# Performance work log

Hardware: AMD Instinct MI355X
Metric: run time of the kernel (lower is better)

Reference implementation:

```python
import jax, jax.numpy as jnp
import numpy as np

B, T, C = 4, 2048, 2048
H, KV, HD = 16, 4, 128  # n_head, n_kv_head, head_dim
G = H // KV             # query heads per kv head


def _rope(t, cos, sin):
    # t: [B, T, h, HD]; cos/sin: [T, HD//2] -> broadcast as [1, T, 1, HD//2]
    tr = t.reshape(t.shape[:-1] + (HD // 2, 2))
    t_r, t_i = tr[..., 0], tr[..., 1]
    c = cos[None, :, None, :]
    s = sin[None, :, None, :]
    o_r = t_r * c - t_i * s
    o_i = t_r * s + t_i * c
    return jnp.stack((o_r, o_i), axis=-1).reshape(t.shape)


def setup_inputs() -> dict:
    key = jax.random.key(0)
    ks = jax.random.split(key, 7)
    sc = 0.02
    return {
        "x": jax.random.normal(ks[0], (B, T, C), jnp.float32),
        "cos_freqs": jnp.cos(jnp.outer(jnp.arange(T, dtype=jnp.float32),
                                       1.0 / (10000.0 ** (jnp.arange(HD // 2, dtype=jnp.float32) * 2 / HD)))),
        "sin_freqs": jnp.sin(jnp.outer(jnp.arange(T, dtype=jnp.float32),
                                       1.0 / (10000.0 ** (jnp.arange(HD // 2, dtype=jnp.float32) * 2 / HD)))),
        "wq": jax.random.normal(ks[1], (H * HD, C), jnp.float32) * sc,
        "wk": jax.random.normal(ks[2], (KV * HD, C), jnp.float32) * sc,
        "wv": jax.random.normal(ks[3], (KV * HD, C), jnp.float32) * sc,
        "wo": jax.random.normal(ks[4], (C, H * HD), jnp.float32) * sc,
    }


def reference(x, cos_freqs, sin_freqs, wq, wk, wv, wo):
    # projections (Linear with bias=False: y = x @ W.T)
    q = (x @ wq.T).reshape(B, T, H, HD)
    k = (x @ wk.T).reshape(B, T, KV, HD)
    v = (x @ wv.T).reshape(B, T, KV, HD)
    q, k = _rope(q, cos_freqs, sin_freqs), _rope(k, cos_freqs, sin_freqs)
    # GQA attention without materializing repeated K/V: group q heads per kv head
    qg = q.reshape(B, T, KV, G, HD).transpose(0, 2, 3, 1, 4)  # [B,KV,G,T,HD]
    kh = k.transpose(0, 2, 1, 3)                              # [B,KV,T,HD]
    vh = v.transpose(0, 2, 1, 3)                              # [B,KV,T,HD]
    scale = 1.0 / jnp.sqrt(jnp.float32(HD))
    scores = jnp.einsum('bkgtd,bksd->bkgts', qg, kh) * scale  # [B,KV,G,T,T]
    mask = jnp.tril(jnp.ones((T, T), dtype=bool))
    scores = jnp.where(mask, scores, jnp.float32(-jnp.inf))
    attn = jax.nn.softmax(scores, axis=-1)
    out = jnp.einsum('bkgts,bksd->bkgtd', attn, vh)           # [B,KV,G,T,HD]
    out = out.transpose(0, 3, 1, 2, 4).reshape(B, T, H * HD)
    return out @ wo.T
```

## Files before the change

### kernel.cpp

```cpp
#include <hip/hip_runtime.h>
#include <hip/hip_bf16.h>
#include <math.h>

typedef __attribute__((ext_vector_type(8))) short short8;
typedef __attribute__((ext_vector_type(4))) float floatx4;

__device__ __forceinline__ float bf2f(unsigned short u) {
  union { unsigned int i; float f; } x; x.i = ((unsigned int)u) << 16; return x.f;
}
__device__ __forceinline__ unsigned short f2bf(float f) {
  union { float f; unsigned int i; } x; x.f = f;
  unsigned int r = x.i + 0x7FFFu + ((x.i >> 16) & 1u);
  return (unsigned short)(r >> 16);
}
__device__ __forceinline__ unsigned int pack2bf(float a, float b) {
  return (unsigned int)f2bf(a) | ((unsigned int)f2bf(b) << 16);
}
__device__ __forceinline__ void gl16(const void* g, void* l) {
  __builtin_amdgcn_global_load_lds(
      (const __attribute__((address_space(1))) unsigned int*)g,
      (__attribute__((address_space(3))) unsigned int*)l, 16, 0, 0);
}
#define BARF  do { __builtin_amdgcn_s_barrier(); asm volatile("" ::: "memory"); } while (0)

__global__ void cvt_f32_bf16(const float* __restrict__ in, unsigned short* __restrict__ out, int n4) {
  int i = blockIdx.x * blockDim.x + threadIdx.x;
  if (i >= n4) return;
  float4 v = ((const float4*)in)[i];
  ushort4 o;
  o.x = f2bf(v.x); o.y = f2bf(v.y); o.z = f2bf(v.z); o.w = f2bf(v.w);
  ((ushort4*)out)[i] = o;
}

template<int MODE>
__global__ __launch_bounds__(512, 2) void gemm_bt(const unsigned short* __restrict__ A,
                                                  const unsigned short* __restrict__ Bw,
                                                  void* __restrict__ out0,
                                                  unsigned short* __restrict__ vtg,
                                                  int M, int N, int K, int nbx) {
  extern __shared__ unsigned short SM[];
  const int nb = gridDim.x;
  const int bid = blockIdx.x;
  const int tile = (bid & 7) * (nb >> 3) + (bid >> 3);
  const int n0 = (tile % nbx) * 256, m0 = (tile / nbx) * 256;
  const int tid = threadIdx.x;
  const int lane = tid & 63, wave = tid >> 6;
  const int wm = wave >> 2, wn = wave & 3;
  const int r = lane & 15, g = lane >> 4;
  const int rh = r >> 1;
  const int slot = (((r & 1) << 2) | g) ^ rh;

  const int sg8 = (tid & 7) ^ ((tid >> 3) & 7);
  const int srow = 2 * (tid >> 3) + (sg8 >> 2);
  const int scol = (sg8 & 3) * 8;
  const unsigned short* Agb = A  + (size_t)(m0 + srow) * K + scol;
  const unsigned short* Bgb = Bw + (size_t)(n0 + srow) * K + scol;
  const size_t K128 = (size_t)K * 128;
  char* const SMb = (char*)SM;

  const int aob = (wm * 64 + rh) * 64 + slot * 8;
  const int bob = 16384 + (wn * 32 + rh) * 64 + slot * 8;

  auto STA = [&](int s, int t, int kh) {
    const unsigned short* gp = Agb + ((size_t)t << 6) + kh * 32;
    char* d = SMb + s * 65536 + kh * 16384 + wave * 1024;
    gl16(gp,        d);
    gl16(gp + K128, d + 8192);
  };
  auto STB = [&](int s, int t, int kh) {
    const unsigned short* gp = Bgb + ((size_t)t << 6) + kh * 32;
    char* d = SMb + s * 65536 + 32768 + kh * 16384 + wave * 1024;
    gl16(gp,        d);
    gl16(gp + K128, d + 8192);
  };

  floatx4 acc[8][4] = {};
  const int NT = K >> 6;

  STA(0, 0, 0); STB(0, 0, 0);
  STA(0, 0, 1); STB(0, 0, 1);
  asm volatile("s_waitcnt vmcnt(0)" ::: "memory");
  __builtin_amdgcn_s_barrier();
  asm volatile("" ::: "memory");

  short8 bfrA[4], afA[4];
#pragma unroll
  for (int j = 0; j < 4; ++j) bfrA[j] = *(const short8*)&SM[bob + j * 512];
#pragma unroll
  for (int i = 0; i < 4; ++i) afA[i] = *(const short8*)&SM[aob + i * 512];

  for (int t = 0; t < NT; ++t) {
    const int s = t & 1;
    const unsigned short* Ls = SM + s * 32768;
    const unsigned short* Ln = SM + (s ^ 1) * 32768;
    const bool pf = (t + 1 < NT);
    short8 afB[4], bfrB[4], afA2[4], afB2[4];

#pragma unroll
    for (int i = 0; i < 4; ++i) afB[i] = *(const short8*)&Ls[aob + (4 + i) * 512];
    if (pf) { STA(s ^ 1, t + 1, 0); STB(s ^ 1, t + 1, 0); }
    __builtin_amdgcn_s_setprio(1);
#pragma unroll
    for (int i = 0; i < 4; ++i)
#pragma unroll
      for (int j = 0; j < 4; ++j)
        acc[i][j] = __builtin_amdgcn_mfma_f32_16x16x32_bf16(afA[i], bfrA[j], acc[i][j], 0, 0, 0);
    __builtin_amdgcn_s_setprio(0);

#pragma unroll
    for (int j = 0; j < 4; ++j) bfrB[j] = *(const short8*)&Ls[bob + 8192 + j * 512];
#pragma unroll
    for (int i = 0; i < 4; ++i) afA2[i] = *(const short8*)&Ls[aob + 8192 + i * 512];
    if (pf) { STA(s ^ 1, t + 1, 1); STB(s ^ 1, t + 1, 1); }
    __builtin_amdgcn_s_setprio(1);
#pragma unroll
    for (int i = 0; i < 4; ++i)
#pragma unroll
      for (int j = 0; j < 4; ++j)
        acc[4 + i][j] = __builtin_amdgcn_mfma_f32_16x16x32_bf16(afB[i], bfrA[j], acc[4 + i][j], 0, 0, 0);
    __builtin_amdgcn_s_setprio(0);

#pragma unroll
    for (int i = 0; i < 4; ++i) afB2[i] = *(const short8*)&Ls[aob + 8192 + (4 + i) * 512];
    __builtin_amdgcn_s_setprio(1);
#pragma unroll
    for (int i = 0; i < 4; ++i)
#pragma unroll
      for (int j = 0; j < 4; ++j)
        acc[i][j] = __builtin_amdgcn_mfma_f32_16x16x32_bf16(afA2[i], bfrB[j], acc[i][j], 0, 0, 0);
    __builtin_amdgcn_s_setprio(0);

    asm volatile("s_waitcnt lgkmcnt(0)" ::: "memory");
    if (pf) asm volatile("s_waitcnt vmcnt(0)" ::: "memory");
    __builtin_amdgcn_s_barrier();
    asm volatile("" ::: "memory");
    if (pf) {
#pragma unroll
      for (int j = 0; j < 4; ++j) bfrA[j] = *(const short8*)&Ln[bob + j * 512];
#pragma unroll
      for (int i = 0; i < 4; ++i) afA[i] = *(const short8*)&Ln[aob + i * 512];
    }
    __builtin_amdgcn_s_setprio(1);
#pragma unroll
    for (int i = 0; i < 4; ++i)
#pragma unroll
      for (int j = 0; j < 4; ++j)
        acc[4 + i][j] = __builtin_amdgcn_mfma_f32_16x16x32_bf16(afB2[i], bfrB[j], acc[4 + i][j], 0, 0, 0);
    __builtin_amdgcn_s_setprio(0);
  }

  if (MODE == 0) {
    float* SMf = (float*)SM;
    float* outp = (float*)out0;
#pragma unroll
    for (int sp = 0; sp < 4; ++sp) {
      __syncthreads();
      if (wn == sp) {
#pragma unroll
        for (int i = 0; i < 8; ++i)
#pragma unroll
          for (int j = 0; j < 4; ++j)
#pragma unroll
            for (int q = 0; q < 4; ++q)
              SMf[(wm * 128 + i * 16 + g * 4 + q) * 64 + j * 16 + r] = acc[i][j][q];
      }
      __syncthreads();
#pragma unroll
      for (int it = 0; it < 8; ++it) {
        int c = it * 512 + tid;
        int ml = c >> 4, c4 = c & 15;
        float4 v = *(float4*)&SMf[ml * 64 + c4 * 4];
        *(float4*)(outp + (size_t)(m0 + ml) * N + n0 + sp * 64 + c4 * 4) = v;
      }
    }
  } else if (n0 < 2560) {
    unsigned short* outp = (unsigned short*)out0;
#pragma unroll
    for (int sp = 0; sp < 2; ++sp) {
      __syncthreads();
      if (wm == sp) {
#pragma unroll
        for (int i = 0; i < 8; ++i)
#pragma unroll
          for (int j = 0; j < 4; ++j)
#pragma unroll
            for (int q = 0; q < 4; ++q)
              SM[(i * 16 + g * 4 + q) * 256 + wn * 64 + j * 16 + r] = f2bf(acc[i][j][q]);
      }
      __syncthreads();
#pragma unroll
      for (int it = 0; it < 8; ++it) {
        int c = it * 512 + tid;
        int ml = c >> 5, c8 = c & 31;
        short8 v = *(short8*)&SM[ml * 256 + c8 * 8];
        *(short8*)(outp + (size_t)(m0 + sp * 128 + ml) * N + n0 + c8 * 8) = v;
      }
    }
  } else {
#pragma unroll
    for (int sp = 0; sp < 8; ++sp) {
      __syncthreads();
      if (wave == sp) {
#pragma unroll
        for (int i = 0; i < 8; ++i)
#pragma unroll
          for (int j = 0; j < 4; ++j)
#pragma unroll
            for (int q = 0; q < 4; ++q) {
              int ml = i * 16 + g * 4 + q;
              int nl = j * 16 + r;
              SM[nl * 128 + (((ml >> 3) ^ (nl & 7)) << 3) + (ml & 7)] = f2bf(acc[i][j][q]);
            }
      }
      __syncthreads();
#pragma unroll
      for (int it = 0; it < 2; ++it) {
        int c = it * 512 + tid;
        int nl = c >> 4, m8 = c & 15;
        short8 v = *(short8*)&SM[nl * 128 + ((m8 ^ (nl & 7)) << 3)];
        *(short8*)(vtg + (size_t)(n0 - 2560 + (sp & 3) * 64 + nl) * 8192 + m0 + (sp >> 2) * 128 + m8 * 8) = v;
      }
    }
  }
}

__global__ void rope_inplace(unsigned short* __restrict__ t,
                             const float* __restrict__ cosf, const float* __restrict__ sinf,
                             int heads, int rowStride, int total, float scale) {
  int i = blockIdx.x * blockDim.x + threadIdx.x;
  if (i >= total) return;
  int d8 = i & 15;
  int rem = i >> 4;
  int head = rem % heads;
  int tok = rem / heads;
  int tpos = tok & 2047;
  unsigned short* p = t + (size_t)tok * rowStride + head * 128 + d8 * 8;
  short8 v = *(short8*)p;
  float4 c = *(const float4*)(cosf + (size_t)tpos * 64 + d8 * 4);
  float4 s = *(const float4*)(sinf + (size_t)tpos * 64 + d8 * 4);
  float cc[4] = {c.x, c.y, c.z, c.w};
  float ss[4] = {s.x, s.y, s.z, s.w};
  short8 o;
#pragma unroll
  for (int j = 0; j < 4; ++j) {
    float tr = bf2f((unsigned short)v[2 * j]);
    float ti = bf2f((unsigned short)v[2 * j + 1]);
    float orr = (tr * cc[j] - ti * ss[j]) * scale;
    float oi  = (tr * ss[j] + ti * cc[j]) * scale;
    o[2 * j]     = (short)f2bf(orr);
    o[2 * j + 1] = (short)f2bf(oi);
  }
  *(short8*)p = o;
}

__global__ __launch_bounds__(256, 2) void attn_fwd(const unsigned short* __restrict__ QKV,
                                                   const unsigned short* __restrict__ VT,
                                                   unsigned short* __restrict__ O) {
  constexpr int T = 2048;
  constexpr int LDQ = 3072;
  constexpr float NEG = -1e30f;
  __shared__ unsigned short Ks[2][64 * 128];
  __shared__ unsigned short Vs[2][128 * 64];
  const int gid = blockIdx.x;
  const int hb  = gid & 63;
  const int qb  = 15 - (gid >> 6);
  const int h = hb & 15, b = hb >> 4;
  const int kvh = h >> 2;
  const int tid = threadIdx.x, lane = tid & 63, w = tid >> 6;
  const int r = lane & 15, g = lane >> 4;
  const int rbase = (r & 3) + ((r >> 2) << 3);
  const int swzr  = (r & 3) | (((r >> 2) & 1) << 2);
  const size_t bT = (size_t)b * T;

  const unsigned short* Kgb = QKV + bT * LDQ + 2048 + kvh * 128;
  const unsigned short* Vgb = VT + (size_t)(kvh * 128) * 8192 + b * 2048;

  auto STAGE = [&](int bi, int kv0) {
#pragma unroll
    for (int t2 = 0; t2 < 4; ++t2) {
      int ck = w * 4 + t2;
      { int row = ck * 4 + (lane >> 4); int c16 = lane & 15;
        int swz = (row & 3) | (((row >> 3) & 1) << 2);
        gl16(Kgb + (size_t)(kv0 + row) * LDQ + ((c16 ^ swz) << 3),
             (char*)(&Ks[bi][0]) + ck * 1024); }
      { int row = ck * 8 + (lane >> 3); int c16 = lane & 7;
        gl16(Vgb + (size_t)row * 8192 + kv0 + ((c16 ^ (row & 7)) << 3),
             (char*)(&Vs[bi][0]) + ck * 1024); }
    }
  };

  const int q0 = qb * 128;

  short8 qf[2][4];
#pragma unroll
  for (int qt = 0; qt < 2; ++qt) {
    const unsigned short* qp = QKV + (bT + q0 + w * 32 + qt * 16 + r) * LDQ + h * 128;
#pragma unroll
    for (int c = 0; c < 4; ++c) qf[qt][c] = *(const short8*)(qp + c * 32 + g * 8);
  }

  floatx4 acc[8][2] = {};
  float mrun[2] = {NEG, NEG};
  float lrun[2] = {0.f, 0.f};

  const int ntiles = (q0 + 128) >> 6;
  STAGE(0, 0);
  asm volatile("s_waitcnt vmcnt(0)" ::: "memory");
  __syncthreads();

  for (int t = 0; t < ntiles; ++t) {
    const int cur = t & 1;
    const int kv0 = t << 6;
    if (t + 1 < ntiles) STAGE(cur ^ 1, (t + 1) << 6);

    if (kv0 <= q0 + w * 32 + 31) {
      floatx4 st[2][4] = {};
      __builtin_amdgcn_s_setprio(1);
#pragma unroll
      for (int c = 0; c < 4; ++c) {
        short8 kf[4];
#pragma unroll
        for (int kt = 0; kt < 4; ++kt) {
          const int row = rbase + ((kt & 1) << 2) + ((kt >> 1) << 5);
          kf[kt] = *(const short8*)&Ks[cur][row * 128 + (((g + 4 * c) ^ swzr) << 3)];
        }
#pragma unroll
        for (int qt = 0; qt < 2; ++qt)
#pragma unroll
          for (int kt = 0; kt < 4; ++kt)
            st[qt][kt] = __builtin_amdgcn_mfma_f32_16x16x32_bf16(kf[kt], qf[qt][c], st[qt][kt], 0, 0, 0);
      }
      __builtin_amdgcn_s_setprio(0);

      short8 va[2][8];
#pragma unroll
      for (int kc = 0; kc < 2; ++kc)
#pragma unroll
        for (int dt = 0; dt < 8; ++dt)
          va[kc][dt] = *(const short8*)&Vs[cur][(dt * 16 + r) * 64 + (((g + 4 * kc) ^ (r & 7)) << 3)];

#pragma unroll
      for (int qt = 0; qt < 2; ++qt) {
        const int qmin = q0 + w * 32 + qt * 16;
        const int qrow = qmin + r;
        float x[4][4];
        bool needmask = (kv0 + 64 > qmin);
#pragma unroll
        for (int kt = 0; kt < 4; ++kt) {
          const int kvb = kv0 + ((kt >> 1) << 5) + (g << 3) + ((kt & 1) << 2);
#pragma unroll
          for (int j = 0; j < 4; ++j) {
            float v = st[qt][kt][j];
            if (needmask) v = (kvb + j <= qrow) ? v : NEG;
            x[kt][j] = v;
          }
        }
        float mloc = x[0][0];
#pragma unroll
        for (int kt = 0; kt < 4; ++kt)
#pragma unroll
          for (int j = 0; j < 4; ++j) mloc = fmaxf(mloc, x[kt][j]);
        mloc = fmaxf(mloc, __shfl_xor(mloc, 16));
        mloc = fmaxf(mloc, __shfl_xor(mloc, 32));
        if (!__all(mloc <= mrun[qt] + 8.f)) {
          float mnew = fmaxf(mrun[qt], mloc);
          float al = __expf(mrun[qt] - mnew);
          mrun[qt] = mnew;
          lrun[qt] *= al;
#pragma unroll
          for (int dt = 0; dt < 8; ++dt) acc[dt][qt] *= al;
        }
        float pr[4][4], ssum = 0.f;
#pragma unroll
        for (int kt = 0; kt < 4; ++kt)
#pragma unroll
          for (int j = 0; j < 4; ++j) { pr[kt][j] = __expf(x[kt][j] - mrun[qt]); ssum += pr[kt][j]; }
        ssum += __shfl_xor(ssum, 16);
        ssum += __shfl_xor(ssum, 32);
        lrun[qt] += ssum;
        uint2 pk[4];
#pragma unroll
        for (int kt = 0; kt < 4; ++kt) {
          pk[kt].x = pack2bf(pr[kt][0], pr[kt][1]);
          pk[kt].y = pack2bf(pr[kt][2], pr[kt][3]);
        }
        __builtin_amdgcn_s_setprio(1);
#pragma unroll
        for (int kc = 0; kc < 2; ++kc) {
          union { unsigned int u[4]; short8 s; } bw;
          bw.u[0] = pk[2 * kc].x;
          bw.u[1] = pk[2 * kc].y;
          bw.u[2] = pk[2 * kc + 1].x;
          bw.u[3] = pk[2 * kc + 1].y;
#pragma unroll
          for (int dt = 0; dt < 8; ++dt)
            acc[dt][qt] = __builtin_amdgcn_mfma_f32_16x16x32_bf16(va[kc][dt], bw.s, acc[dt][qt], 0, 0, 0);
        }
        __builtin_amdgcn_s_setprio(0);
      }
    }

    asm volatile("s_waitcnt vmcnt(0)" ::: "memory");
    __syncthreads();
  }

#pragma unroll
  for (int qt = 0; qt < 2; ++qt) {
    float inv = 1.f / lrun[qt];
    unsigned short* op = O + (bT + q0 + w * 32 + qt * 16 + r) * 2048 + h * 128;
#pragma unroll
    for (int dt = 0; dt < 8; ++dt) {
      uint2 pkd;
      pkd.x = pack2bf(acc[dt][qt][0] * inv, acc[dt][qt][1] * inv);
      pkd.y = pack2bf(acc[dt][qt][2] * inv, acc[dt][qt][3] * inv);
      *(uint2*)(op + dt * 16 + g * 4) = pkd;
    }
  }
}

extern "C" void kernel_launch(void* const* d_in, const int* in_sizes, int n_in,
                              void* d_out, int out_size, void* d_ws, size_t ws_size,
                              hipStream_t stream) {
  const float* x    = (const float*)d_in[0];
  const float* cosf = (const float*)d_in[1];
  const float* sinf = (const float*)d_in[2];
  const float* wq   = (const float*)d_in[3];
  const float* wk   = (const float*)d_in[4];
  const float* wv   = (const float*)d_in[5];
  const float* wo   = (const float*)d_in[6];

  unsigned short* xb   = (unsigned short*)d_ws;
  unsigned short* qkvw = xb   + 16777216;
  unsigned short* wob  = qkvw + 6291456;
  unsigned short* qkv  = wob  + 4194304;
  unsigned short* Vtg  = qkv  + 25165824;
  unsigned short* AO   = Vtg  + 4194304;

  static int _attr_once = []() {
    hipFuncSetAttribute((const void*)gemm_bt<0>, hipFuncAttributeMaxDynamicSharedMemorySize, 131072);
    hipFuncSetAttribute((const void*)gemm_bt<1>, hipFuncAttributeMaxDynamicSharedMemorySize, 131072);
    return 0;
  }();
  (void)_attr_once;

  cvt_f32_bf16<<<16384, 256, 0, stream>>>(x,  xb,  4194304);
  cvt_f32_bf16<<<4096,  256, 0, stream>>>(wq, qkvw,           1048576);
  cvt_f32_bf16<<<1024,  256, 0, stream>>>(wk, qkvw + 4194304, 262144);
  cvt_f32_bf16<<<1024,  256, 0, stream>>>(wv, qkvw + 5242880, 262144);
  cvt_f32_bf16<<<4096,  256, 0, stream>>>(wo, wob, 1048576);

  gemm_bt<1><<<384, 512, 131072, stream>>>(xb, qkvw, qkv, Vtg, 8192, 3072, 2048, 12);

  rope_inplace<<<8192, 256, 0, stream>>>(qkv,        cosf, sinf, 16, 3072, 2097152, 0.08838834764831845f);
  rope_inplace<<<2048, 256, 0, stream>>>(qkv + 2048, cosf, sinf, 4,  3072, 524288,  1.0f);

  attn_fwd<<<1024, 256, 0, stream>>>(qkv, Vtg, AO);

  gemm_bt<0><<<256, 512, 131072, stream>>>(AO, wob, d_out, nullptr, 8192, 2048, 2048, 8);
}
```

Measured before the change: 361.6 us.

## Add 128x128-tile GEMM kernel for QKV projection to improve CU occupancy

Adds a new 128x128-tile bf16 GEMM kernel with 256 threads, double-buffered LDS staging via global_load_lds, and a split MFMA schedule. The QKV projection now uses it with 1536 blocks instead of 384 blocks of 256x256 tiles. The aim is to fill the GPU's compute units more evenly, since 384 large tiles leave a poor last wave on 256 CUs. The cost is more global/LDS traffic per FLOP from the smaller tiles. The output projection keeps the old 256-tile kernel, which is renamed.

```diff
diff --git a/kernel.cpp b/kernel.cpp
--- a/kernel.cpp
+++ b/kernel.cpp
@@ -21,7 +21,6 @@
       (const __attribute__((address_space(1))) unsigned int*)g,
       (__attribute__((address_space(3))) unsigned int*)l, 16, 0, 0);
 }
-#define BARF  do { __builtin_amdgcn_s_barrier(); asm volatile("" ::: "memory"); } while (0)
 
 __global__ void cvt_f32_bf16(const float* __restrict__ in, unsigned short* __restrict__ out, int n4) {
   int i = blockIdx.x * blockDim.x + threadIdx.x;
@@ -33,7 +32,178 @@
 }
 
 template<int MODE>
-__global__ __launch_bounds__(512, 2) void gemm_bt(const unsigned short* __restrict__ A,
+__global__ __launch_bounds__(256, 3) void gemm128(const unsigned short* __restrict__ A,
+                                                  const unsigned short* __restrict__ Bw,
+                                                  void* __restrict__ out0,
+                                                  unsigned short* __restrict__ vtg,
+                                                  int M, int N, int K, int nbx) {
+  __shared__ __align__(16) unsigned short SM[16384];
+  const int nb = gridDim.x;
+  const int bid = blockIdx.x;
+  const int tile = (bid & 7) * (nb >> 3) + (bid >> 3);
+  const int n0 = (tile % nbx) * 128, m0 = (tile / nbx) * 128;
+  const int tid = threadIdx.x;
+  const int lane = tid & 63, wave = tid >> 6;
+  const int wm = wave >> 1, wn = wave & 1;
+  const int r = lane & 15, g = lane >> 4;
+  const int swzr = (r >> 1) & 3;
+
+  const int scg = (tid & 3) ^ ((tid >> 3) & 3);
+  const unsigned short* Arow = A  + (size_t)(m0 + (tid >> 2)) * K + scg * 8;
+  const unsigned short* Brow = Bw + (size_t)(n0 + (tid >> 2)) * K + scg * 8;
+  const size_t K64 = (size_t)K * 64;
+  char* const Lw = (char*)SM + wave * 1024;
+
+  const int aoff = (wm * 64 + r) * 32 + ((g ^ swzr) << 3);
+  const int boff = 4096 + (wn * 64 + r) * 32 + ((g ^ swzr) << 3);
+
+  auto STAGE = [&](int slot, int t) {
+    const unsigned short* Ag = Arow + ((size_t)t << 5);
+    const unsigned short* Bg = Brow + ((size_t)t << 5);
+    char* L = Lw + slot * 16384;
+    gl16(Ag,       L);
+    gl16(Ag + K64, L + 4096);
+    gl16(Bg,       L + 8192);
+    gl16(Bg + K64, L + 12288);
+  };
+
+  floatx4 acc[4][4] = {};
+  const int NT = K >> 5;
+
+  STAGE(0, 0);
+  asm volatile("s_waitcnt vmcnt(0)" ::: "memory");
+  __builtin_amdgcn_s_barrier();
+  asm volatile("" ::: "memory");
+
+  short8 bf[4], af01[2];
+#pragma unroll
+  for (int j = 0; j < 4; ++j) bf[j] = *(const short8*)&SM[boff + j * 512];
+#pragma unroll
+  for (int k = 0; k < 2; ++k) af01[k] = *(const short8*)&SM[aoff + k * 512];
+
+  for (int t = 0; t < NT; ++t) {
+    const int s = t & 1;
+    const unsigned short* Ls = SM + s * 8192;
+    const unsigned short* Ln = SM + (s ^ 1) * 8192;
+    const bool pf = (t + 1 < NT);
+    short8 af23[2], bfN[4], afN[2];
+
+#pragma unroll
+    for (int k = 0; k < 2; ++k) af23[k] = *(const short8*)&Ls[aoff + (2 + k) * 512];
+    if (pf) STAGE(s ^ 1, t + 1);
+    __builtin_amdgcn_s_setprio(1);
+#pragma unroll
+    for (int j = 0; j < 4; ++j) {
+      acc[0][j] = __builtin_amdgcn_mfma_f32_16x16x32_bf16(af01[0], bf[j], acc[0][j], 0, 0, 0);
+      acc[1][j] = __builtin_amdgcn_mfma_f32_16x16x32_bf16(af01[1], bf[j], acc[1][j], 0, 0, 0);
+    }
+    __builtin_amdgcn_s_setprio(0);
+
+    asm volatile("s_waitcnt lgkmcnt(0)" ::: "memory");
+    if (pf) asm volatile("s_waitcnt vmcnt(0)" ::: "memory");
+    __builtin_amdgcn_s_barrier();
+    asm volatile("" ::: "memory");
+    if (pf) {
+#pragma unroll
+      for (int j = 0; j < 4; ++j) bfN[j] = *(const short8*)&Ln[boff + j * 512];
+#pragma unroll
+      for (int k = 0; k < 2; ++k) afN[k] = *(const short8*)&Ln[aoff + k * 512];
+    }
+    __builtin_amdgcn_s_setprio(1);
+#pragma unroll
+    for (int j = 0; j < 4; ++j) {
+      acc[2][j] = __builtin_amdgcn_mfma_f32_16x16x32_bf16(af23[0], bf[j], acc[2][j], 0, 0, 0);
+      acc[3][j] = __builtin_amdgcn_mfma_f32_16x16x32_bf16(af23[1], bf[j], acc[3][j], 0, 0, 0);
+    }
+    __builtin_amdgcn_s_setprio(0);
+    if (pf) {
+#pragma unroll
+      for (int j = 0; j < 4; ++j) bf[j] = bfN[j];
+      af01[0] = afN[0]; af01[1] = afN[1];
+    }
+  }
+
+  if (MODE == 0) {
+    float* SMf = (float*)SM;
+    float* outp = (float*)out0;
+#pragma unroll
+    for (int p = 0; p < 4; ++p) {
+      __syncthreads();
+      if (wm == (p >> 1)) {
+#pragma unroll
+        for (int i2 = 0; i2 < 2; ++i2) {
+          int i = (p & 1) * 2 + i2;
+#pragma unroll
+          for (int j = 0; j < 4; ++j)
+#pragma unroll
+            for (int q = 0; q < 4; ++q)
+              SMf[(i2 * 16 + g * 4 + q) * 128 + wn * 64 + j * 16 + r] = acc[i][j][q];
+        }
+      }
+      __syncthreads();
+#pragma unroll
+      for (int it = 0; it < 4; ++it) {
+        int c = it * 256 + tid;
+        int row = c >> 5, c4 = c & 31;
+        float4 v = *(float4*)&SMf[row * 128 + c4 * 4];
+        *(float4*)(outp + (size_t)(m0 + p * 32 + row) * N + n0 + c4 * 4) = v;
+      }
+    }
+  } else if (n0 < 2560) {
+    unsigned short* outp = (unsigned short*)out0;
+#pragma unroll
+    for (int p = 0; p < 4; ++p) {
+      __syncthreads();
+      if (wm == (p >> 1)) {
+#pragma unroll
+        for (int i2 = 0; i2 < 2; ++i2) {
+          int i = (p & 1) * 2 + i2;
+#pragma unroll
+          for (int j = 0; j < 4; ++j)
+#pragma unroll
+            for (int q = 0; q < 4; ++q)
+              SM[(i2 * 16 + g * 4 + q) * 128 + wn * 64 + j * 16 + r] = f2bf(acc[i][j][q]);
+        }
+      }
+      __syncthreads();
+#pragma unroll
+      for (int it = 0; it < 2; ++it) {
+        int c = it * 256 + tid;
+        int row = c >> 4, c8 = c & 15;
+        short8 v = *(short8*)&SM[row * 128 + c8 * 8];
+        *(short8*)(outp + (size_t)(m0 + p * 32 + row) * N + n0 + c8 * 8) = v;
+      }
+    }
+  } else {
+#pragma unroll
+    for (int p = 0; p < 2; ++p) {
+      __syncthreads();
+      if (wn == p) {
+#pragma unroll
+        for (int i = 0; i < 4; ++i)
+#pragma unroll
+          for (int j = 0; j < 4; ++j)
+#pragma unroll
+            for (int q = 0; q < 4; ++q) {
+              int ml = wm * 64 + i * 16 + g * 4 + q;
+              int nl = j * 16 + r;
+              SM[nl * 128 + (((ml >> 3) ^ (nl & 7)) << 3) + (ml & 7)] = f2bf(acc[i][j][q]);
+            }
+      }
+      __syncthreads();
+#pragma unroll
+      for (int it = 0; it < 4; ++it) {
+        int c = it * 256 + tid;
+        int nl = c >> 4, m8 = c & 15;
+        short8 v = *(short8*)&SM[nl * 128 + ((m8 ^ (nl & 7)) << 3)];
+        *(short8*)(vtg + (size_t)(n0 - 2560 + p * 64 + nl) * 8192 + m0 + m8 * 8) = v;
+      }
+    }
+  }
+}
+
+template<int MODE>
+__global__ __launch_bounds__(512, 2) void gemm256(const unsigned short* __restrict__ A,
                                                   const unsigned short* __restrict__ Bw,
                                                   void* __restrict__ out0,
                                                   unsigned short* __restrict__ vtg,
@@ -437,8 +607,7 @@
   unsigned short* AO   = Vtg  + 4194304;
 
   static int _attr_once = []() {
-    hipFuncSetAttribute((const void*)gemm_bt<0>, hipFuncAttributeMaxDynamicSharedMemorySize, 131072);
-    hipFuncSetAttribute((const void*)gemm_bt<1>, hipFuncAttributeMaxDynamicSharedMemorySize, 131072);
+    hipFuncSetAttribute((const void*)gemm256<0>, hipFuncAttributeMaxDynamicSharedMemorySize, 131072);
     return 0;
   }();
   (void)_attr_once;
@@ -449,12 +618,12 @@
   cvt_f32_bf16<<<1024,  256, 0, stream>>>(wv, qkvw + 5242880, 262144);
   cvt_f32_bf16<<<4096,  256, 0, stream>>>(wo, wob, 1048576);
 
-  gemm_bt<1><<<384, 512, 131072, stream>>>(xb, qkvw, qkv, Vtg, 8192, 3072, 2048, 12);
+  gemm128<1><<<1536, 256, 0, stream>>>(xb, qkvw, qkv, Vtg, 8192, 3072, 2048, 24);
 
   rope_inplace<<<8192, 256, 0, stream>>>(qkv,        cosf, sinf, 16, 3072, 2097152, 0.08838834764831845f);
   rope_inplace<<<2048, 256, 0, stream>>>(qkv + 2048, cosf, sinf, 4,  3072, 524288,  1.0f);
 
   attn_fwd<<<1024, 256, 0, stream>>>(qkv, Vtg, AO);
 
-  gemm_bt<0><<<256, 512, 131072, stream>>>(AO, wob, d_out, nullptr, 8192, 2048, 2048, 8);
-}
+  gemm256<0><<<256, 512, 131072, stream>>>(AO, wob, d_out, nullptr, 8192, 2048, 2048, 8);
+}
```

Result: slower. 373.5 us (+3.3%).
